# Kernel optimization log

Measured on AMD Instinct MI355X. Metric: run time of the kernel, lower is better.

The kernel has to match this reference:

```python
import jax, jax.numpy as jnp
import numpy as np

B, N, K_OUT, NBASIS, NGLOBALS, H = 16, 2048, 128, 4, 2, 256
DIN = 1 + NBASIS + N + NGLOBALS  # norm + basis projections + all-pairs dots + globals
NEG_SLOPE = 0.01  # torch LeakyReLU default


def setup_inputs() -> dict:
    key = jax.random.key(0)
    ks = jax.random.split(key, 6)
    x = jax.random.uniform(ks[0], (B, N, 3), jnp.float32)      # positions -> dots >= 0
    u = jax.random.normal(ks[1], (B, NGLOBALS), jnp.float32)
    basis = jax.random.normal(ks[2], (B, NBASIS, 3), jnp.float32)
    def init_w(k, fan_in, fan_out):
        return jax.random.normal(k, (fan_in, fan_out), jnp.float32) / np.float32(np.sqrt(fan_in))
    W1 = init_w(ks[3], DIN, H); b1 = jnp.zeros((H,), jnp.float32)
    W2 = init_w(ks[4], H, H);   b2 = jnp.zeros((H,), jnp.float32)
    W3 = init_w(ks[5], H, K_OUT); b3 = jnp.zeros((K_OUT,), jnp.float32)
    return {"x": x, "u": u, "basis": basis,
            "W1": W1, "b1": b1, "W2": W2, "b2": b2, "W3": W3, "b3": b3}


def reference(x, u, basis, W1, b1, W2, b2, W3, b3):
    # per-vector norms: [B, N, 1]
    norms = jnp.linalg.norm(x, axis=-1, keepdims=True)
    # projections onto basis vectors: [B, N, NBASIS]
    proj = jnp.einsum('bid,bnd->bin', x, basis)
    # all-pairs sqrt of dot products: [B, N, N]
    dots = jnp.sqrt(jnp.einsum('bid,bjd->bij', x, x))
    # concat order matches original: globals first, then [norm, proj, dots]
    u_rep = jnp.broadcast_to(u[:, None, :], (B, N, NGLOBALS))
    scalars = jnp.concatenate([u_rep, norms, proj, dots], axis=-1)  # [B, N, DIN]
    # MLP (Linear -> LeakyReLU -> Linear -> LeakyReLU -> Linear)
    h = jax.nn.leaky_relu(scalars @ W1 + b1, NEG_SLOPE)
    h = jax.nn.leaky_relu(h @ W2 + b2, NEG_SLOPE)
    fk = h @ W3 + b3  # [B, N, K_OUT]
    # outer product with x followed by mean over input vecs, fused into one einsum
    # (avoids materializing the [B, N, K_OUT, 3] tensor)
    return jnp.einsum('bio,bid->bod', fk, x) / np.float32(N)  # [B, K_OUT, 3]
```

## Files before the change

kernel.cpp:

```cpp
#include <hip/hip_runtime.h>

typedef unsigned short u16;
typedef unsigned int   u32;

typedef __attribute__((ext_vector_type(8))) short short8;
typedef __attribute__((ext_vector_type(4))) float floatx4;
typedef __attribute__((ext_vector_type(2))) float v2f;

__device__ __forceinline__ u16 f2bf(float f) {
    u32 u = __float_as_uint(f);
    u = u + 0x7fffu + ((u >> 16) & 1u);
    return (u16)(u >> 16);
}

__device__ __forceinline__ u32 pack2bf(float s0, float s1) {
    u32 a = __float_as_uint(s0) + 0x8000u;
    u32 b = __float_as_uint(s1) + 0x8000u;
    return __builtin_amdgcn_perm(b, a, 0x07060302u);
}

__device__ __forceinline__ floatx4 mfma16(short8 a, short8 b, floatx4 c) {
    return __builtin_amdgcn_mfma_f32_16x16x32_bf16(a, b, c, 0, 0, 0);
}

__global__ void k_prep(const float* __restrict__ x, const float* __restrict__ W1,
                       const float* __restrict__ W2, const float* __restrict__ W3,
                       float* __restrict__ xsoa, u16* __restrict__ W1frag,
                       u16* __restrict__ W2frag, u16* __restrict__ W3frag,
                       float* __restrict__ out) {
    int idx = blockIdx.x * 256 + threadIdx.x;
    if (idx < 6144) out[idx] = 0.f;
    if (idx < 98304) {
        int b = idx / 6144, r = idx - b * 6144;
        int comp = r >> 11, n = r & 2047;
        xsoa[idx] = x[(b * 2048 + n) * 3 + comp];
    } else if (idx < 622592) {
        int i = idx - 98304;
        int row = i >> 8, c = i & 255;
        float v = W1[1792 + i];
        int kt = row >> 5, rr = row & 31;
        int lq = rr >> 3, ji = rr & 7;
        int w = c >> 5, cc = c & 31;
        int j = cc >> 4, lr = cc & 15;
        W1frag[kt * 8192 + (w * 64 + lq * 16 + lr) * 16 + j * 8 + ji] = f2bf(v);
    } else if (idx < 688128) {
        int i = idx - 622592;
        int row = i >> 8, c = i & 255;
        float v = W2[i];
        int kt = row >> 5, rr = row & 31;
        int lq = rr >> 3, ji = rr & 7;
        int w = c >> 5, cc = c & 31;
        int j = cc >> 4, lr = cc & 15;
        W2frag[kt * 8192 + (w * 64 + lq * 16 + lr) * 16 + j * 8 + ji] = f2bf(v);
    } else if (idx < 720896) {
        int i = idx - 688128;
        int row = i >> 7, c = i & 127;
        float v = W3[i];
        int kt = row >> 5, rr = row & 31;
        int lq = rr >> 3, ji = rr & 7;
        int w = c >> 4, lr = c & 15;
        W3frag[kt * 4096 + (w * 64 + lq * 16 + lr) * 8 + ji] = f2bf(v);
    }
}

__global__ __launch_bounds__(512, 4) void k_fused(
    const float* __restrict__ xsoa, const float* __restrict__ u,
    const float* __restrict__ basis, const float* __restrict__ W1,
    const float* __restrict__ b1, const float* __restrict__ b2,
    const float* __restrict__ b3, const u16* __restrict__ W1frag,
    const u16* __restrict__ W2frag, const u16* __restrict__ W3frag,
    float* __restrict__ out) {
    __shared__ __align__(16) char smem[76288];
    char* Asb = smem + 24576;
    u16 (*h1s)[264] = (u16(*)[264])smem;
    float (*xsm)[4] = (float(*)[4])(smem + 33792);
    float (*redm)[4] = (float(*)[4])(smem + 34816);
    float (*rowsml)[6] = (float(*)[6])(smem + 40960);
    float (*colsml)[8] = (float(*)[8])(smem + 42496);
    u16 (*h2s)[264] = (u16(*)[264])(smem + 42496);

    const int t = threadIdx.x;
    const int b = blockIdx.y;
    const int i0 = blockIdx.x * 64;
    const int lane = t & 63, w = t >> 6;
    const int lr = lane & 15, lq = lane >> 4;

    const float* Xg = xsoa + b * 6144;
    const float ax = Xg[i0 + lane];
    const float ay = Xg[2048 + i0 + lane];
    const float az = Xg[4096 + i0 + lane];

    if (t < 256) {
        int c = t;
        float u0 = u[b * 2 + 0], u1 = u[b * 2 + 1];
        colsml[c][0] = b1[c] + u0 * W1[c] + u1 * W1[256 + c];
        colsml[c][1] = W1[512 + c];
        colsml[c][2] = W1[768 + c];
        colsml[c][3] = W1[1024 + c];
        colsml[c][4] = W1[1280 + c];
        colsml[c][5] = W1[1536 + c];
        colsml[c][6] = b2[c];
        if (c < 128) colsml[c][7] = b3[c];
    }
    if (t < 64) {
        rowsml[t][0] = sqrtf(ax * ax + ay * ay + az * az);
#pragma unroll
        for (int p = 0; p < 4; ++p) {
            const float* bp = basis + (b * 4 + p) * 3;
            rowsml[t][1 + p] = ax * bp[0] + ay * bp[1] + az * bp[2];
        }
    }

    char* aswp = Asb + lane * 128 + ((w ^ (lane & 7)) << 4);
    int ro[4];
    {
        int sl = (lq ^ (lr & 7));
#pragma unroll
        for (int i = 0; i < 4; ++i)
            ro[i] = (i * 16 + lr) * 128 + (sl << 4);
    }

    struct XR { float4 x0, x1, y0, y1, z0, z1; };
    auto gen_load = [&](int s) {
        int c0u = __builtin_amdgcn_readfirstlane(s * 64 + w * 8);
        const float* Xc = Xg + c0u;
        XR r;
        r.x0 = *(const float4*)(Xc);        r.x1 = *(const float4*)(Xc + 4);
        r.y0 = *(const float4*)(Xc + 2048); r.y1 = *(const float4*)(Xc + 2052);
        r.z0 = *(const float4*)(Xc + 4096); r.z1 = *(const float4*)(Xc + 4100);
        return r;
    };
    auto gen_cs = [&](const XR& rg, int buf) {
        v2f dA, dB, dC, dD;
        {
            v2f t0 = {rg.x0.x, rg.x0.y}, t1 = {rg.x0.z, rg.x0.w};
            v2f t2 = {rg.x1.x, rg.x1.y}, t3 = {rg.x1.z, rg.x1.w};
            dA = t0 * ax; dB = t1 * ax; dC = t2 * ax; dD = t3 * ax;
        }
        {
            v2f t0 = {rg.y0.x, rg.y0.y}, t1 = {rg.y0.z, rg.y0.w};
            v2f t2 = {rg.y1.x, rg.y1.y}, t3 = {rg.y1.z, rg.y1.w};
            dA += t0 * ay; dB += t1 * ay; dC += t2 * ay; dD += t3 * ay;
        }
        {
            v2f t0 = {rg.z0.x, rg.z0.y}, t1 = {rg.z0.z, rg.z0.w};
            v2f t2 = {rg.z1.x, rg.z1.y}, t3 = {rg.z1.z, rg.z1.w};
            dA += t0 * az; dB += t1 * az; dC += t2 * az; dD += t3 * az;
        }
        float s0 = __builtin_amdgcn_sqrtf(dA.x);
        float s1 = __builtin_amdgcn_sqrtf(dA.y);
        float s2 = __builtin_amdgcn_sqrtf(dB.x);
        float s3 = __builtin_amdgcn_sqrtf(dB.y);
        float s4 = __builtin_amdgcn_sqrtf(dC.x);
        float s5 = __builtin_amdgcn_sqrtf(dC.y);
        float s6 = __builtin_amdgcn_sqrtf(dD.x);
        float s7 = __builtin_amdgcn_sqrtf(dD.y);
        uint4 dv;
        dv.x = pack2bf(s0, s1); dv.y = pack2bf(s2, s3);
        dv.z = pack2bf(s4, s5); dv.w = pack2bf(s6, s7);
        *(uint4*)(aswp + buf * 8192) = dv;
    };

    floatx4 acc[4][2];
    const floatx4 zero = {0.f, 0.f, 0.f, 0.f};
#pragma unroll
    for (int i = 0; i < 4; ++i)
#pragma unroll
        for (int j = 0; j < 2; ++j) acc[i][j] = zero;

    {
        XR r0 = gen_load(0);
        gen_cs(r0, 0);
    }
    XR R = gen_load(1);
    __syncthreads();

    {
        const u16* wf = W1frag + t * 16;
        short8 a[4], bfr[4];
#pragma unroll 2
        for (int s = 0; s < 32; ++s) {
            const int buf = s & 1;
            const u16* wb = wf + (2 * s) * 8192;
            bfr[0] = *(const short8*)(wb);
            bfr[1] = *(const short8*)(wb + 8);
            bfr[2] = *(const short8*)(wb + 8192);
            bfr[3] = *(const short8*)(wb + 8192 + 8);
#pragma unroll
            for (int i = 0; i < 4; ++i)
                a[i] = *(const short8*)(Asb + buf * 8192 + ro[i]);
            if (s < 31) gen_cs(R, buf ^ 1);
            if (s < 30) R = gen_load(s + 2);
#pragma unroll
            for (int i = 0; i < 4; ++i)
#pragma unroll
                for (int j = 0; j < 2; ++j)
                    acc[i][j] = mfma16(a[i], bfr[j], acc[i][j]);
#pragma unroll
            for (int i = 0; i < 4; ++i)
                a[i] = *(const short8*)(Asb + buf * 8192 + (ro[i] ^ 64));
#pragma unroll
            for (int i = 0; i < 4; ++i)
#pragma unroll
                for (int j = 0; j < 2; ++j)
                    acc[i][j] = mfma16(a[i], bfr[2 + j], acc[i][j]);
            __syncthreads();
        }
    }

    if (t < 64) { xsm[t][0] = ax; xsm[t][1] = ay; xsm[t][2] = az; }
    const int c0 = w * 32 + lr, c1 = c0 + 16;
    const int c3 = w * 16 + lr;
    float cb0, cb1, cb3;
    {
        float c0v[7], c1v[7];
#pragma unroll
        for (int q = 0; q < 7; ++q) { c0v[q] = colsml[c0][q]; c1v[q] = colsml[c1][q]; }
        cb0 = c0v[6]; cb1 = c1v[6];
        cb3 = colsml[c3][7];
#pragma unroll
        for (int i = 0; i < 4; ++i) {
#pragma unroll
            for (int r = 0; r < 4; ++r) {
                int row = i * 16 + lq * 4 + r;
                float nrm = rowsml[row][0];
                float p0 = rowsml[row][1], p1 = rowsml[row][2];
                float p2 = rowsml[row][3], p3 = rowsml[row][4];
                float v0 = acc[i][0][r] + c0v[0] + nrm * c0v[1] +
                           p0 * c0v[2] + p1 * c0v[3] + p2 * c0v[4] + p3 * c0v[5];
                v0 = v0 > 0.f ? v0 : 0.01f * v0;
                h1s[row][c0] = f2bf(v0);
                float v1 = acc[i][1][r] + c1v[0] + nrm * c1v[1] +
                           p0 * c1v[2] + p1 * c1v[3] + p2 * c1v[4] + p3 * c1v[5];
                v1 = v1 > 0.f ? v1 : 0.01f * v1;
                h1s[row][c1] = f2bf(v1);
            }
        }
    }
    __syncthreads();

#pragma unroll
    for (int i = 0; i < 4; ++i)
#pragma unroll
        for (int j = 0; j < 2; ++j) acc[i][j] = zero;
    {
        const u16* w2s = W2frag + t * 16;
#pragma unroll 2
        for (int kt = 0; kt < 8; ++kt) {
            short8 af[4], bfr[2];
#pragma unroll
            for (int i = 0; i < 4; ++i)
                af[i] = *(const short8*)&h1s[i * 16 + lr][kt * 32 + lq * 8];
#pragma unroll
            for (int j = 0; j < 2; ++j)
                bfr[j] = *(const short8*)(w2s + kt * 8192 + j * 8);
#pragma unroll
            for (int i = 0; i < 4; ++i)
#pragma unroll
                for (int j = 0; j < 2; ++j)
                    acc[i][j] = mfma16(af[i], bfr[j], acc[i][j]);
        }
#pragma unroll
        for (int i = 0; i < 4; ++i)
#pragma unroll
            for (int r = 0; r < 4; ++r) {
                int row = i * 16 + lq * 4 + r;
                float v0 = acc[i][0][r] + cb0;
                v0 = v0 > 0.f ? v0 : 0.01f * v0;
                h2s[row][c0] = f2bf(v0);
                float v1 = acc[i][1][r] + cb1;
                v1 = v1 > 0.f ? v1 : 0.01f * v1;
                h2s[row][c1] = f2bf(v1);
            }
    }
    __syncthreads();

    {
        floatx4 acc2[4];
#pragma unroll
        for (int i = 0; i < 4; ++i) acc2[i] = zero;
        const u16* w3s = W3frag + t * 8;
#pragma unroll 2
        for (int kt = 0; kt < 8; ++kt) {
            short8 af[4];
#pragma unroll
            for (int i = 0; i < 4; ++i)
                af[i] = *(const short8*)&h2s[i * 16 + lr][kt * 32 + lq * 8];
            short8 bfr = *(const short8*)(w3s + kt * 4096);
#pragma unroll
            for (int i = 0; i < 4; ++i) acc2[i] = mfma16(af[i], bfr, acc2[i]);
        }
        float s0 = 0.f, s1 = 0.f, s2 = 0.f;
#pragma unroll
        for (int i = 0; i < 4; ++i)
#pragma unroll
            for (int r = 0; r < 4; ++r) {
                int row = i * 16 + lq * 4 + r;
                float fk = acc2[i][r] + cb3;
                s0 += fk * xsm[row][0];
                s1 += fk * xsm[row][1];
                s2 += fk * xsm[row][2];
            }
        s0 += __shfl_xor(s0, 16); s0 += __shfl_xor(s0, 32);
        s1 += __shfl_xor(s1, 16); s1 += __shfl_xor(s1, 32);
        s2 += __shfl_xor(s2, 16); s2 += __shfl_xor(s2, 32);
        if (lq == 0) {
            redm[c3][0] = s0; redm[c3][1] = s1; redm[c3][2] = s2;
        }
    }
    __syncthreads();
    if (t < 128) {
#pragma unroll
        for (int d = 0; d < 3; ++d)
            atomicAdd(&out[(b * 128 + t) * 3 + d], redm[t][d] * (1.0f / 2048.0f));
    }
}

extern "C" void kernel_launch(void* const* d_in, const int* in_sizes, int n_in,
                              void* d_out, int out_size, void* d_ws, size_t ws_size,
                              hipStream_t stream) {
    const float* x     = (const float*)d_in[0];
    const float* u     = (const float*)d_in[1];
    const float* basis = (const float*)d_in[2];
    const float* W1    = (const float*)d_in[3];
    const float* b1    = (const float*)d_in[4];
    const float* W2    = (const float*)d_in[5];
    const float* b2    = (const float*)d_in[6];
    const float* W3    = (const float*)d_in[7];
    const float* b3    = (const float*)d_in[8];
    float* out = (float*)d_out;

    char* ws = (char*)d_ws;
    u16*  W1frag = (u16*)ws;
    u16*  W2frag = (u16*)(ws + 1048576);
    u16*  W3frag = (u16*)(ws + 1179648);
    float* xsoa  = (float*)(ws + 1245184);

    k_prep<<<2816, 256, 0, stream>>>(x, W1, W2, W3, xsoa, W1frag, W2frag,
                                     W3frag, out);
    k_fused<<<dim3(32, 16), 512, 0, stream>>>(xsoa, u, basis, W1, b1, b2, b3,
                                              W1frag, W2frag, W3frag, out);
}
```

Baseline: 123.9 us.

## Halve rows per block to 32, shrink LDS, reuse h1 buffer for h2

Each block now handles 32 rows instead of 64, which doubles the grid to 1024 blocks and halves the per-wave accumulator tiles. Shared memory drops from about 76KB to 28KB by aliasing the A staging buffer with h1 and writing h2 back into h1 after an extra barrier. Launch bounds rise to 6 waves per SIMD to raise occupancy and spread work across more CUs. The cost is that every W1, W2 and W3 fragment now feeds half as many rows, so global weight traffic per row doubles. Half-wave lanes also produce half-width dot-product chunks.

```diff
diff --git a/kernel.cpp b/kernel.cpp
--- a/kernel.cpp
+++ b/kernel.cpp
@@ -63,32 +63,32 @@
     }
 }
 
-__global__ __launch_bounds__(512, 4) void k_fused(
+__global__ __launch_bounds__(512, 6) void k_fused(
     const float* __restrict__ xsoa, const float* __restrict__ u,
     const float* __restrict__ basis, const float* __restrict__ W1,
     const float* __restrict__ b1, const float* __restrict__ b2,
     const float* __restrict__ b3, const u16* __restrict__ W1frag,
     const u16* __restrict__ W2frag, const u16* __restrict__ W3frag,
     float* __restrict__ out) {
-    __shared__ __align__(16) char smem[76288];
-    char* Asb = smem + 24576;
+    __shared__ __align__(16) char smem[28416];
+    char* Asb = smem;
     u16 (*h1s)[264] = (u16(*)[264])smem;
-    float (*xsm)[4] = (float(*)[4])(smem + 33792);
-    float (*redm)[4] = (float(*)[4])(smem + 34816);
-    float (*rowsml)[6] = (float(*)[6])(smem + 40960);
-    float (*colsml)[8] = (float(*)[8])(smem + 42496);
-    u16 (*h2s)[264] = (u16(*)[264])(smem + 42496);
+    float (*xsm)[4] = (float(*)[4])(smem + 16896);
+    float (*redm)[4] = (float(*)[4])(smem + 17408);
+    float (*rowsml)[6] = (float(*)[6])(smem + 19456);
+    float (*colsml)[8] = (float(*)[8])(smem + 20224);
 
     const int t = threadIdx.x;
     const int b = blockIdx.y;
-    const int i0 = blockIdx.x * 64;
+    const int i0 = blockIdx.x * 32;
     const int lane = t & 63, w = t >> 6;
     const int lr = lane & 15, lq = lane >> 4;
+    const int row32 = lane & 31, hi = lane >> 5;
 
     const float* Xg = xsoa + b * 6144;
-    const float ax = Xg[i0 + lane];
-    const float ay = Xg[2048 + i0 + lane];
-    const float az = Xg[4096 + i0 + lane];
+    const float ax = Xg[i0 + row32];
+    const float ay = Xg[2048 + i0 + row32];
+    const float az = Xg[4096 + i0 + row32];
 
     if (t < 256) {
         int c = t;
@@ -102,21 +102,22 @@
         colsml[c][6] = b2[c];
         if (c < 128) colsml[c][7] = b3[c];
     }
-    if (t < 64) {
+    if (t < 32) {
         rowsml[t][0] = sqrtf(ax * ax + ay * ay + az * az);
 #pragma unroll
         for (int p = 0; p < 4; ++p) {
             const float* bp = basis + (b * 4 + p) * 3;
             rowsml[t][1 + p] = ax * bp[0] + ay * bp[1] + az * bp[2];
         }
-    }
-
-    char* aswp = Asb + lane * 128 + ((w ^ (lane & 7)) << 4);
-    int ro[4];
+        xsm[t][0] = ax; xsm[t][1] = ay; xsm[t][2] = az;
+    }
+
+    char* aswp = Asb + row32 * 128 + ((w ^ (row32 & 7)) << 4) + hi * 8;
+    int ro[2];
     {
         int sl = (lq ^ (lr & 7));
 #pragma unroll
-        for (int i = 0; i < 4; ++i)
+        for (int i = 0; i < 2; ++i)
             ro[i] = (i * 16 + lr) * 128 + (sl << 4);
     }
 
@@ -131,40 +132,35 @@
         return r;
     };
     auto gen_cs = [&](const XR& rg, int buf) {
-        v2f dA, dB, dC, dD;
+        float4 xa = hi ? rg.x1 : rg.x0;
+        float4 ya = hi ? rg.y1 : rg.y0;
+        float4 za = hi ? rg.z1 : rg.z0;
+        v2f dA, dB;
         {
-            v2f t0 = {rg.x0.x, rg.x0.y}, t1 = {rg.x0.z, rg.x0.w};
-            v2f t2 = {rg.x1.x, rg.x1.y}, t3 = {rg.x1.z, rg.x1.w};
-            dA = t0 * ax; dB = t1 * ax; dC = t2 * ax; dD = t3 * ax;
+            v2f t0 = {xa.x, xa.y}, t1 = {xa.z, xa.w};
+            dA = t0 * ax; dB = t1 * ax;
         }
         {
-            v2f t0 = {rg.y0.x, rg.y0.y}, t1 = {rg.y0.z, rg.y0.w};
-            v2f t2 = {rg.y1.x, rg.y1.y}, t3 = {rg.y1.z, rg.y1.w};
-            dA += t0 * ay; dB += t1 * ay; dC += t2 * ay; dD += t3 * ay;
+            v2f t0 = {ya.x, ya.y}, t1 = {ya.z, ya.w};
+            dA += t0 * ay; dB += t1 * ay;
         }
         {
-            v2f t0 = {rg.z0.x, rg.z0.y}, t1 = {rg.z0.z, rg.z0.w};
-            v2f t2 = {rg.z1.x, rg.z1.y}, t3 = {rg.z1.z, rg.z1.w};
-            dA += t0 * az; dB += t1 * az; dC += t2 * az; dD += t3 * az;
+            v2f t0 = {za.x, za.y}, t1 = {za.z, za.w};
+            dA += t0 * az; dB += t1 * az;
         }
         float s0 = __builtin_amdgcn_sqrtf(dA.x);
         float s1 = __builtin_amdgcn_sqrtf(dA.y);
         float s2 = __builtin_amdgcn_sqrtf(dB.x);
         float s3 = __builtin_amdgcn_sqrtf(dB.y);
-        float s4 = __builtin_amdgcn_sqrtf(dC.x);
-        float s5 = __builtin_amdgcn_sqrtf(dC.y);
-        float s6 = __builtin_amdgcn_sqrtf(dD.x);
-        float s7 = __builtin_amdgcn_sqrtf(dD.y);
-        uint4 dv;
+        uint2 dv;
         dv.x = pack2bf(s0, s1); dv.y = pack2bf(s2, s3);
-        dv.z = pack2bf(s4, s5); dv.w = pack2bf(s6, s7);
-        *(uint4*)(aswp + buf * 8192) = dv;
+        *(uint2*)(aswp + buf * 4096) = dv;
     };
 
-    floatx4 acc[4][2];
+    floatx4 acc[2][2];
     const floatx4 zero = {0.f, 0.f, 0.f, 0.f};
 #pragma unroll
-    for (int i = 0; i < 4; ++i)
+    for (int i = 0; i < 2; ++i)
 #pragma unroll
         for (int j = 0; j < 2; ++j) acc[i][j] = zero;
 
@@ -177,7 +173,7 @@
 
     {
         const u16* wf = W1frag + t * 16;
-        short8 a[4], bfr[4];
+        short8 a[2], bfr[4];
 #pragma unroll 2
         for (int s = 0; s < 32; ++s) {
             const int buf = s & 1;
@@ -187,20 +183,20 @@
             bfr[2] = *(const short8*)(wb + 8192);
             bfr[3] = *(const short8*)(wb + 8192 + 8);
 #pragma unroll
-            for (int i = 0; i < 4; ++i)
-                a[i] = *(const short8*)(Asb + buf * 8192 + ro[i]);
+            for (int i = 0; i < 2; ++i)
+                a[i] = *(const short8*)(Asb + buf * 4096 + ro[i]);
             if (s < 31) gen_cs(R, buf ^ 1);
             if (s < 30) R = gen_load(s + 2);
 #pragma unroll
-            for (int i = 0; i < 4; ++i)
+            for (int i = 0; i < 2; ++i)
 #pragma unroll
                 for (int j = 0; j < 2; ++j)
                     acc[i][j] = mfma16(a[i], bfr[j], acc[i][j]);
 #pragma unroll
-            for (int i = 0; i < 4; ++i)
-                a[i] = *(const short8*)(Asb + buf * 8192 + (ro[i] ^ 64));
-#pragma unroll
-            for (int i = 0; i < 4; ++i)
+            for (int i = 0; i < 2; ++i)
+                a[i] = *(const short8*)(Asb + buf * 4096 + (ro[i] ^ 64));
+#pragma unroll
+            for (int i = 0; i < 2; ++i)
 #pragma unroll
                 for (int j = 0; j < 2; ++j)
                     acc[i][j] = mfma16(a[i], bfr[2 + j], acc[i][j]);
@@ -208,7 +204,6 @@
         }
     }
 
-    if (t < 64) { xsm[t][0] = ax; xsm[t][1] = ay; xsm[t][2] = az; }
     const int c0 = w * 32 + lr, c1 = c0 + 16;
     const int c3 = w * 16 + lr;
     float cb0, cb1, cb3;
@@ -219,7 +214,7 @@
         cb0 = c0v[6]; cb1 = c1v[6];
         cb3 = colsml[c3][7];
 #pragma unroll
-        for (int i = 0; i < 4; ++i) {
+        for (int i = 0; i < 2; ++i) {
 #pragma unroll
             for (int r = 0; r < 4; ++r) {
                 int row = i * 16 + lq * 4 + r;
@@ -240,59 +235,60 @@
     __syncthreads();
 
 #pragma unroll
-    for (int i = 0; i < 4; ++i)
+    for (int i = 0; i < 2; ++i)
 #pragma unroll
         for (int j = 0; j < 2; ++j) acc[i][j] = zero;
     {
         const u16* w2s = W2frag + t * 16;
 #pragma unroll 2
         for (int kt = 0; kt < 8; ++kt) {
-            short8 af[4], bfr[2];
-#pragma unroll
-            for (int i = 0; i < 4; ++i)
+            short8 af[2], bfr[2];
+#pragma unroll
+            for (int i = 0; i < 2; ++i)
                 af[i] = *(const short8*)&h1s[i * 16 + lr][kt * 32 + lq * 8];
 #pragma unroll
             for (int j = 0; j < 2; ++j)
                 bfr[j] = *(const short8*)(w2s + kt * 8192 + j * 8);
 #pragma unroll
-            for (int i = 0; i < 4; ++i)
+            for (int i = 0; i < 2; ++i)
 #pragma unroll
                 for (int j = 0; j < 2; ++j)
                     acc[i][j] = mfma16(af[i], bfr[j], acc[i][j]);
         }
-#pragma unroll
-        for (int i = 0; i < 4; ++i)
-#pragma unroll
-            for (int r = 0; r < 4; ++r) {
-                int row = i * 16 + lq * 4 + r;
-                float v0 = acc[i][0][r] + cb0;
-                v0 = v0 > 0.f ? v0 : 0.01f * v0;
-                h2s[row][c0] = f2bf(v0);
-                float v1 = acc[i][1][r] + cb1;
-                v1 = v1 > 0.f ? v1 : 0.01f * v1;
-                h2s[row][c1] = f2bf(v1);
-            }
-    }
-    __syncthreads();
-
-    {
-        floatx4 acc2[4];
-#pragma unroll
-        for (int i = 0; i < 4; ++i) acc2[i] = zero;
+    }
+    __syncthreads();
+#pragma unroll
+    for (int i = 0; i < 2; ++i)
+#pragma unroll
+        for (int r = 0; r < 4; ++r) {
+            int row = i * 16 + lq * 4 + r;
+            float v0 = acc[i][0][r] + cb0;
+            v0 = v0 > 0.f ? v0 : 0.01f * v0;
+            h1s[row][c0] = f2bf(v0);
+            float v1 = acc[i][1][r] + cb1;
+            v1 = v1 > 0.f ? v1 : 0.01f * v1;
+            h1s[row][c1] = f2bf(v1);
+        }
+    __syncthreads();
+
+    {
+        floatx4 acc2[2];
+#pragma unroll
+        for (int i = 0; i < 2; ++i) acc2[i] = zero;
         const u16* w3s = W3frag + t * 8;
 #pragma unroll 2
         for (int kt = 0; kt < 8; ++kt) {
-            short8 af[4];
-#pragma unroll
-            for (int i = 0; i < 4; ++i)
-                af[i] = *(const short8*)&h2s[i * 16 + lr][kt * 32 + lq * 8];
+            short8 af[2];
+#pragma unroll
+            for (int i = 0; i < 2; ++i)
+                af[i] = *(const short8*)&h1s[i * 16 + lr][kt * 32 + lq * 8];
             short8 bfr = *(const short8*)(w3s + kt * 4096);
 #pragma unroll
-            for (int i = 0; i < 4; ++i) acc2[i] = mfma16(af[i], bfr, acc2[i]);
+            for (int i = 0; i < 2; ++i) acc2[i] = mfma16(af[i], bfr, acc2[i]);
         }
         float s0 = 0.f, s1 = 0.f, s2 = 0.f;
 #pragma unroll
-        for (int i = 0; i < 4; ++i)
+        for (int i = 0; i < 2; ++i)
 #pragma unroll
             for (int r = 0; r < 4; ++r) {
                 int row = i * 16 + lq * 4 + r;
@@ -338,6 +334,6 @@
 
     k_prep<<<2816, 256, 0, stream>>>(x, W1, W2, W3, xsoa, W1frag, W2frag,
                                      W3frag, out);
-    k_fused<<<dim3(32, 16), 512, 0, stream>>>(xsoa, u, basis, W1, b1, b2, b3,
+    k_fused<<<dim3(64, 16), 512, 0, stream>>>(xsoa, u, basis, W1, b1, b2, b3,
                                               W1frag, W2frag, W3frag, out);
 }
```

Result: slower. 143.7 us (+16.0%).
